# Kernel tuning notes

Hardware: AMD Instinct MI355X
Metric: run time of the kernel (lower is better)

## Reference

```python
import jax, jax.numpy as jnp
from jax import lax
import numpy as np

V, D, L, E = 32000, 256, 4, 4
B, S = 1, 4096  # B must be 1: AstroNorm's buffer update/broadcast only works for batch==1
SIG = float(1.0 / (1.0 + np.exp(-0.15)))        # sigmoid(init_sparsity=0.15), static (int() detaches)
K_GATE = max(1, int(S * SIG))                    # tokens kept by sparsity gate
K_EXP = max(1, int(0.8 * E))                     # int(sparsity_constraint * num_experts) = 3


def setup_inputs() -> dict:
    key = jax.random.key(0)
    ks = jax.random.split(key, 8)
    s = 0.02
    return {
        "tokens": jax.random.randint(ks[0], (B, S), 0, V),
        "emb": jax.random.normal(ks[1], (V, D)) * s,
        "buffers": jax.random.normal(ks[2], (L, D)) * 0.1,   # AstroNorm buffer per layer
        "decays": jnp.full((L,), 0.95),                       # AstroNorm decay per layer
        "gate_w": jax.random.normal(ks[3], (L, D)) * s,       # context_gate (Linear(dim,1,bias=False))
        "gating_W": jax.random.normal(ks[4], (L, E, D)) * s,  # expert router
        "gating_b": jnp.zeros((L, E)),
        "exp_W": jax.random.normal(ks[5], (L, E, D, D)) * s,  # per-expert Linear(dim,dim)
        "exp_b": jnp.zeros((L, E, D)),
        "ln_g": jnp.ones((D,)),
        "ln_b": jnp.zeros((D,)),
        "head_W": jax.random.normal(ks[6], (V, D)) * s,
        "head_b": jnp.zeros((V,)),
    }


def _forward(tokens, emb, buffers, decays, gate_w, gating_W, gating_b,
             exp_W, exp_b, ln_g, ln_b, head_W, head_b):
    x = emb[tokens]  # [B,S,D]
    for l in range(L):
        # ---- AstroNorm: stats over sequence dim (dim=1), detached as in torch ----
        mu = lax.stop_gradient(jnp.mean(x, axis=1, keepdims=True))           # [B,1,D]
        var = lax.stop_gradient(jnp.var(x, axis=1, keepdims=True, ddof=1))   # unbiased var
        new_buf = decays[l] * buffers[l] + (1.0 - decays[l]) * mu.squeeze()  # [D] (B==1)
        x = jnp.where(jnp.abs(x - mu) > jnp.abs(new_buf), mu, x) / jnp.sqrt(var + 1e-6)
        # ---- DynamicSparsityGate: keep tokens strictly above k-th score ----
        scores = jnp.einsum('bsd,d->bs', x, gate_w[l])
        thr = lax.top_k(scores, K_GATE)[0][:, -1:]           # k-th largest per row
        x = x * (scores > thr).astype(x.dtype)[..., None]
        # ---- SparseExpert: top-K_EXP experts per token, masked accumulation ----
        gs = jnp.einsum('bsd,ed->bse', x, gating_W[l]) + gating_b[l]
        idx = lax.top_k(gs, K_EXP)[1]                                    # [B,S,k]
        emask = (jax.nn.one_hot(idx, E).sum(-2) > 0).astype(x.dtype)     # [B,S,E]
        ys = jnp.einsum('bsd,eod->bseo', x, exp_W[l]) + exp_b[l]         # all-expert outputs
        x = jnp.einsum('bse,bseo->bso', emask, ys)
    # ---- LayerNorm (biased var, eps=1e-5) + vocab head ----
    mu = jnp.mean(x, axis=-1, keepdims=True)
    v = jnp.var(x, axis=-1, keepdims=True)
    x = (x - mu) / jnp.sqrt(v + 1e-5) * ln_g + ln_b
    return jnp.einsum('bsd,vd->bsv', x, head_W) + head_b


def reference(tokens, emb, buffers, decays, gate_w, gating_W, gating_b,
              exp_W, exp_b, ln_g, ln_b, head_W, head_b):
    return _forward(tokens, emb, buffers, decays, gate_w, gating_W, gating_b,
                    exp_W, exp_b, ln_g, ln_b, head_W, head_b)
```

## Files before the change

### kernel.cpp

```cpp
#include <hip/hip_runtime.h>
#include <hip/hip_bf16.h>
#include <math.h>

#define V 32000
#define D 256
#define L 4
#define E 4
#define S 4096
#define K_GATE 2201
#define NE 1024
#define NCH 64
#define SCHUNK 64
#define CTS 136


typedef __hip_bfloat16 bf16;
typedef __attribute__((ext_vector_type(8))) short bf16x8;
typedef __attribute__((ext_vector_type(4))) float f32x4;

__device__ __forceinline__ float loadf(const void* p, size_t i, int bf) {
    if (bf) return __bfloat162float(((const bf16*)p)[i]);
    return ((const float*)p)[i];
}

#define GLDS16(g, l)                                                            \
    __builtin_amdgcn_global_load_lds(                                           \
        (const __attribute__((address_space(1))) unsigned int*)(g),             \
        (__attribute__((address_space(3))) unsigned int*)(l), 16, 0, 0)

__device__ __forceinline__ void stage_tile(const bf16* __restrict__ src, int rowStride,
                                           short* lds, int t, int k0) {
    int w = t >> 6, l = t & 63;
    #pragma unroll
    for (int i = 0; i < 2; i++) {
        int chunk = (w * 2 + i) * 64 + l;
        int row = chunk >> 2;
        int c8 = (chunk & 3) ^ ((row >> 1) & 3);
        const bf16* g = src + (size_t)row * rowStride + k0 + c8 * 8;
        GLDS16(g, (char*)lds + (size_t)(w * 2 + i) * 1024);
    }
}

__device__ __forceinline__ bf16x8 frag_ld(const short* lds, int row, int quad) {
    return *(const bf16x8*)&lds[row * 32 + ((quad ^ ((row >> 1) & 3)) << 3)];
}

__global__ void k_detect(const void* __restrict__ emb, int* __restrict__ flag) {
    const unsigned short* h = (const unsigned short*)emb;
    int cnt = 0;
    for (int i = 0; i < 128; i += 2) {
        int e = (h[i] >> 7) & 0xFF;
        if (e >= 100 && e <= 130) cnt++;
    }
    *flag = (cnt >= 32) ? 1 : 0;
}

__global__ void k_wcast(const void* __restrict__ W, const int* __restrict__ bfp,
                        bf16* __restrict__ Wb) {
    if (*bfp) return;
    size_t idx = ((size_t)blockIdx.x * 256 + threadIdx.x) * 4;
    float4 v = *(const float4*)((const float*)W + idx);
    Wb[idx + 0] = __float2bfloat16(v.x);
    Wb[idx + 1] = __float2bfloat16(v.y);
    Wb[idx + 2] = __float2bfloat16(v.z);
    Wb[idx + 3] = __float2bfloat16(v.w);
}

__global__ void k_embed(const int* __restrict__ tok, const void* __restrict__ emb,
                        const int* __restrict__ bfp, float* __restrict__ x) {
    int s = blockIdx.x, d = threadIdx.x;
    int bf = *bfp;
    int t = tok[s];
    x[s * D + d] = loadf(emb, (size_t)t * D + d, bf);
}

__global__ void k_stats_part(const float* __restrict__ x, float* __restrict__ psum,
                             float* __restrict__ psq) {
    int b = blockIdx.x;
    int t = threadIdx.x;
    float s = 0.f, q = 0.f;
    int s0 = b * SCHUNK;
    #pragma unroll 4
    for (int i = 0; i < SCHUNK; i++) {
        float v = x[(size_t)(s0 + i) * D + t];
        s += v; q += v * v;
    }
    psum[b * D + t] = s;
    psq[b * D + t] = q;
}

__global__ void k_stats_fin(const float* __restrict__ psum, const float* __restrict__ psq,
                            const void* __restrict__ buffers, const void* __restrict__ decays,
                            const int* __restrict__ bfp, int l,
                            float* __restrict__ mu, float* __restrict__ rstd,
                            float* __restrict__ absnb) {
    int t = threadIdx.x;
    int bf = *bfp;
    float s = 0.f, q = 0.f;
    for (int b = 0; b < NCH; b++) { s += psum[b * D + t]; q += psq[b * D + t]; }
    float m = s / (float)S;
    float var = (q - (float)S * m * m) / (float)(S - 1);
    float dec = loadf(decays, l, bf);
    float nb = dec * loadf(buffers, l * D + t, bf) + (1.f - dec) * m;
    mu[t] = m;
    rstd[t] = rsqrtf(var + 1e-6f);
    absnb[t] = fabsf(nb);
}

__global__ void k_norm_score(float* __restrict__ x, const float* __restrict__ mu,
                             const float* __restrict__ rstd, const float* __restrict__ absnb,
                             const void* __restrict__ gate_w, const int* __restrict__ bfp,
                             int l, float* __restrict__ scores) {
    int t = threadIdx.x, w = t >> 6, ln = t & 63;
    int s = blockIdx.x * 4 + w;
    int bf = *bfp;
    float part = 0.f;
    #pragma unroll
    for (int j = 0; j < 4; j++) {
        int f = ln + j * 64;
        float m = mu[f];
        float v = x[(size_t)s * D + f];
        float xv = (fabsf(v - m) > absnb[f]) ? m : v;
        xv *= rstd[f];
        x[(size_t)s * D + f] = xv;
        part += xv * loadf(gate_w, l * D + f, bf);
    }
    #pragma unroll
    for (int m2 = 1; m2 < 64; m2 <<= 1) part += __shfl_xor(part, m2, 64);
    if (ln == 0) scores[s] = part;
}

__global__ void k_thr(const float* __restrict__ scores, float* __restrict__ thr) {
    __shared__ unsigned keys[S];
    __shared__ unsigned hist[256];
    __shared__ unsigned scanb[256];
    __shared__ unsigned sh_pref, sh_rank, sh_bucket;
    int t = threadIdx.x;
    for (int i = t; i < S; i += 256) {
        unsigned u = __float_as_uint(scores[i]);
        keys[i] = (u & 0x80000000u) ? ~u : (u | 0x80000000u);
    }
    if (t == 0) { sh_pref = 0u; sh_rank = S - K_GATE; }
    __syncthreads();
    for (int shift = 24; shift >= 0; shift -= 8) {
        unsigned pref = sh_pref, r = sh_rank;
        unsigned pmask = (shift == 24) ? 0u : (0xFFFFFFFFu << (shift + 8));
        hist[t] = 0u;
        __syncthreads();
        for (int i = t; i < S; i += 256) {
            unsigned k = keys[i];
            if ((k & pmask) == pref) atomicAdd(&hist[(k >> shift) & 0xFF], 1u);
        }
        __syncthreads();
        unsigned v = hist[t];
        scanb[t] = v;
        __syncthreads();
        for (int o = 1; o < 256; o <<= 1) {
            unsigned u2 = (t >= o) ? scanb[t - o] : 0u;
            __syncthreads();
            scanb[t] += u2;
            __syncthreads();
        }
        unsigned incl = scanb[t], exc = incl - v;
        if (exc <= r && r < incl) {
            sh_bucket = t;
            sh_rank = r - exc;
        }
        __syncthreads();
        if (t == 0) sh_pref = pref | (sh_bucket << shift);
        __syncthreads();
    }
    if (t == 0) {
        unsigned k = sh_pref;
        unsigned u = (k & 0x80000000u) ? (k ^ 0x80000000u) : ~k;
        thr[0] = __uint_as_float(u);
    }
}

__global__ void k_route(const float* __restrict__ x, const float* __restrict__ scores,
                        const float* __restrict__ thr,
                        const void* __restrict__ gating_W, const void* __restrict__ gating_b,
                        const int* __restrict__ bfp, int l,
                        float* __restrict__ xg, int* __restrict__ excl) {
    int t = threadIdx.x, w = t >> 6, ln = t & 63;
    int s = blockIdx.x * 4 + w;
    int bf = *bfp;
    float keep = (scores[s] > thr[0]) ? 1.f : 0.f;
    float xv[4];
    #pragma unroll
    for (int j = 0; j < 4; j++) {
        int f = ln + j * 64;
        float v = x[(size_t)s * D + f] * keep;
        xv[j] = v;
        xg[(size_t)s * D + f] = v;
    }
    float gs[E];
    #pragma unroll
    for (int e = 0; e < E; e++) {
        float p = 0.f;
        #pragma unroll
        for (int j = 0; j < 4; j++)
            p += xv[j] * loadf(gating_W, (size_t)(l * E + e) * D + ln + j * 64, bf);
        #pragma unroll
        for (int m2 = 1; m2 < 64; m2 <<= 1) p += __shfl_xor(p, m2, 64);
        gs[e] = p + loadf(gating_b, l * E + e, bf);
    }
    if (ln == 0) {
        int mi = 0; float mv = gs[0];
        #pragma unroll
        for (int e = 1; e < E; e++) if (gs[e] <= mv) { mv = gs[e]; mi = e; }
        excl[s] = mi;
    }
}

#define BM 64
#define BN 64
#define BK 32
__global__ __launch_bounds__(256) void k_egemm(const float* __restrict__ xg,
                                               const void* __restrict__ exp_W,
                                               const int* __restrict__ bfp, int l,
                                               float* __restrict__ Y) {
    __shared__ float As[BK][BM + 1];
    __shared__ float Bs[BK][BN + 1];
    int bf = *bfp;
    int bn = blockIdx.x * BN;
    int bm = blockIdx.y * BM;
    int t = threadIdx.x;
    int tm = (t >> 4) << 2;
    int tn = (t & 15) << 2;
    float acc[4][4] = {};
    for (int k0 = 0; k0 < D; k0 += BK) {
        for (int i = t; i < BM * BK; i += 256) {
            int m = i >> 5, k = i & 31;
            As[k][m] = xg[(size_t)(bm + m) * D + k0 + k];
        }
        for (int i = t; i < BN * BK; i += 256) {
            int n = i >> 5, k = i & 31;
            int gn = bn + n;
            int e = gn >> 8, o = gn & 255;
            Bs[k][n] = loadf(exp_W, ((size_t)((l * E + e) * D + o)) * D + k0 + k, bf);
        }
        __syncthreads();
        for (int k = 0; k < BK; k++) {
            float a[4], bb[4];
            #pragma unroll
            for (int i = 0; i < 4; i++) a[i] = As[k][tm + i];
            #pragma unroll
            for (int j = 0; j < 4; j++) bb[j] = Bs[k][tn + j];
            #pragma unroll
            for (int i = 0; i < 4; i++)
                #pragma unroll
                for (int j = 0; j < 4; j++)
                    acc[i][j] += a[i] * bb[j];
        }
        __syncthreads();
    }
    #pragma unroll
    for (int i = 0; i < 4; i++)
        #pragma unroll
        for (int j = 0; j < 4; j++)
            Y[(size_t)(bm + tm + i) * NE + bn + tn + j] = acc[i][j];
}

__global__ void k_combine(const float* __restrict__ Y, const int* __restrict__ excl,
                          const void* __restrict__ exp_b, const int* __restrict__ bfp,
                          int l, float* __restrict__ xo) {
    int s = blockIdx.x, t = threadIdx.x;
    int bf = *bfp;
    int ex = excl[s];
    float a = 0.f;
    for (int e = 0; e < E; e++) {
        if (e == ex) continue;
        a += Y[(size_t)s * NE + e * D + t] + loadf(exp_b, (size_t)(l * E + e) * D + t, bf);
    }
    xo[s * D + t] = a;
}

__global__ void k_ln(const float* __restrict__ x, const void* __restrict__ g,
                     const void* __restrict__ b, const int* __restrict__ bfp,
                     bf16* __restrict__ xnb) {
    int t = threadIdx.x, w = t >> 6, ln = t & 63;
    int s = blockIdx.x * 4 + w;
    int bf = *bfp;
    float vv[4];
    float sum = 0.f, sq = 0.f;
    #pragma unroll
    for (int j = 0; j < 4; j++) {
        float v = x[(size_t)s * D + ln + j * 64];
        vv[j] = v; sum += v; sq += v * v;
    }
    #pragma unroll
    for (int m2 = 1; m2 < 64; m2 <<= 1) {
        sum += __shfl_xor(sum, m2, 64);
        sq  += __shfl_xor(sq, m2, 64);
    }
    float m = sum / (float)D;
    float var = sq / (float)D - m * m;
    float r = rsqrtf(var + 1e-5f);
    #pragma unroll
    for (int j = 0; j < 4; j++) {
        int f = ln + j * 64;
        xnb[(size_t)s * D + f] = __float2bfloat16((vv[j] - m) * r * loadf(g, f, bf)
                                                  + loadf(b, f, bf));
    }
}

__global__ __launch_bounds__(256) void k_head_mfma(const bf16* __restrict__ xnb,
                                                   const void* __restrict__ head_W_raw,
                                                   const bf16* __restrict__ Wb,
                                                   const void* __restrict__ bias,
                                                   const int* __restrict__ bfp,
                                                   void* __restrict__ out) {
    __shared__ __align__(16) char smem[128 * CTS * 2];
    short* At = (short*)smem;
    short* Bt = (short*)(smem + 8192);
    short* Ct = (short*)smem;
    int bf = *bfp;
    const bf16* Wsrc = bf ? (const bf16*)head_W_raw : Wb;
    int bs = blockIdx.x * 128;
    int bv = blockIdx.y * 128;
    int t = threadIdx.x;
    int wave = t >> 6, lane = t & 63;
    int wm = (wave >> 1) * 64, wn = (wave & 1) * 64;
    int quad = lane >> 4, l16 = lane & 15;

    f32x4 acc[4][4] = {};
    for (int k0 = 0; k0 < D; k0 += 32) {
        stage_tile(xnb + (size_t)bs * D, D, At, t, k0);
        stage_tile(Wsrc + (size_t)bv * D, D, Bt, t, k0);
        __syncthreads();
        bf16x8 af[4], bfg[4];
        #pragma unroll
        for (int i = 0; i < 4; i++) af[i]  = frag_ld(At, wm + i * 16 + l16, quad);
        #pragma unroll
        for (int j = 0; j < 4; j++) bfg[j] = frag_ld(Bt, wn + j * 16 + l16, quad);
        #pragma unroll
        for (int i = 0; i < 4; i++)
            #pragma unroll
            for (int j = 0; j < 4; j++)
                acc[i][j] = __builtin_amdgcn_mfma_f32_16x16x32_bf16(af[i], bfg[j], acc[i][j], 0, 0, 0);
        __syncthreads();
    }
    if (bf) {
        #pragma unroll
        for (int j = 0; j < 4; j++) {
            int colL = wn + j * 16 + l16;
            float bb = __bfloat162float(((const bf16*)bias)[bv + colL]);
            #pragma unroll
            for (int i = 0; i < 4; i++) {
                int rowL = wm + i * 16 + quad * 4;
                #pragma unroll
                for (int rg = 0; rg < 4; rg++) {
                    bf16 hv = __float2bfloat16(acc[i][j][rg] + bb);
                    Ct[(rowL + rg) * CTS + colL] = *(short*)&hv;
                }
            }
        }
        __syncthreads();
        bf16* ob = (bf16*)out;
        #pragma unroll
        for (int k = 0; k < 8; k++) {
            int cc = k * 256 + t;
            int row = cc >> 4, c16 = cc & 15;
            bf16x8 v = *(const bf16x8*)&Ct[row * CTS + c16 * 8];
            *(bf16x8*)(ob + (size_t)(bs + row) * V + bv + c16 * 8) = v;
        }
    } else {
        float* of = (float*)out;
        #pragma unroll
        for (int j = 0; j < 4; j++) {
            int col = bv + wn + j * 16 + l16;
            float bb = loadf(bias, col, bf);
            #pragma unroll
            for (int i = 0; i < 4; i++) {
                int row0 = bs + wm + i * 16 + quad * 4;
                #pragma unroll
                for (int rg = 0; rg < 4; rg++)
                    of[(size_t)(row0 + rg) * V + col] = acc[i][j][rg] + bb;
            }
        }
    }
}

extern "C" void kernel_launch(void* const* d_in, const int* in_sizes, int n_in,
                              void* d_out, int out_size, void* d_ws, size_t ws_size,
                              hipStream_t stream) {
    const int*  tokens   = (const int*)d_in[0];
    const void* emb      = d_in[1];
    const void* buffers  = d_in[2];
    const void* decays   = d_in[3];
    const void* gate_w   = d_in[4];
    const void* gating_W = d_in[5];
    const void* gating_b = d_in[6];
    const void* exp_W    = d_in[7];
    const void* exp_b    = d_in[8];
    const void* ln_g     = d_in[9];
    const void* ln_b     = d_in[10];
    const void* head_W   = d_in[11];
    const void* head_b   = d_in[12];

    char* p = (char*)d_ws;
    bf16* Wb    = (bf16*)p;             p += (size_t)V * D * 2;
    bf16* xnb   = (bf16*)p;             p += (size_t)S * D * 2;
    float* xA   = (float*)p;            p += (size_t)S * D * 4;
    float* xB   = (float*)p;            p += (size_t)S * D * 4;
    float* xg   = (float*)p;            p += (size_t)S * D * 4;
    float* Y    = (float*)p;            p += (size_t)S * NE * 4;
    float* psum = (float*)p;            p += (size_t)NCH * D * 4;
    float* psq  = (float*)p;            p += (size_t)NCH * D * 4;
    float* scores = (float*)p;          p += (size_t)S * 4;
    float* mu   = (float*)p;            p += D * 4;
    float* rstd = (float*)p;            p += D * 4;
    float* absnb = (float*)p;           p += D * 4;
    float* thr  = (float*)p;            p += 16;
    int* flag   = (int*)p;              p += 16;
    int* excl   = (int*)p;              p += (size_t)S * 4;

    k_detect<<<1, 1, 0, stream>>>(emb, flag);
    k_wcast<<<(V * D) / 1024, 256, 0, stream>>>(head_W, flag, Wb);
    k_embed<<<S, D, 0, stream>>>(tokens, emb, flag, xA);

    float* xc = xA;
    float* xo = xB;
    for (int l = 0; l < L; l++) {
        k_stats_part<<<NCH, 256, 0, stream>>>(xc, psum, psq);
        k_stats_fin<<<1, 256, 0, stream>>>(psum, psq, buffers, decays, flag, l, mu, rstd, absnb);
        k_norm_score<<<S / 4, 256, 0, stream>>>(xc, mu, rstd, absnb, gate_w, flag, l, scores);
        k_thr<<<1, 256, 0, stream>>>(scores, thr);
        k_route<<<S / 4, 256, 0, stream>>>(xc, scores, thr, gating_W, gating_b, flag, l,
                                           xg, excl);
        dim3 ge(NE / BN, S / BM);
        k_egemm<<<ge, 256, 0, stream>>>(xg, exp_W, flag, l, Y);
        k_combine<<<S, 256, 0, stream>>>(Y, excl, exp_b, flag, l, xo);
        float* tmp = xc; xc = xo; xo = tmp;
    }
    k_ln<<<S / 4, 256, 0, stream>>>(xc, ln_g, ln_b, flag, xnb);
    dim3 gh(S / 128, V / 128);
    k_head_mfma<<<gh, 256, 0, stream>>>(xnb, head_W, Wb, head_b, flag, d_out);
}
```

Measured before the change: 1.180 ms.

## Fuse routing into expert GEMM and combine, enlarge GEMM tiles, speed up threshold select

Removes the separate routing kernel. The sparsity mask is now applied while staging A tiles in the expert GEMM, and the router logits plus excluded-expert choice are computed inside the combine kernel, which drops the xg and excl buffers and one launch per layer. The FP32 expert GEMM moves from 64x64 to 128x128 tiles with 8x8 per-thread outputs and vectorized loads and stores, raising arithmetic intensity at the cost of more registers and fewer blocks. The radix threshold kernel now runs 1024 threads and replaces the barrier-heavy shared-memory scan with a single-wave shuffle scan.

Result: faster. 991.7 us (-16.0%).

```diff
diff --git a/kernel.cpp b/kernel.cpp
--- a/kernel.cpp
+++ b/kernel.cpp
@@ -22,6 +22,9 @@
     if (bf) return __bfloat162float(((const bf16*)p)[i]);
     return ((const float*)p)[i];
 }
+__device__ __forceinline__ float us2f(unsigned short u) {
+    return __uint_as_float((unsigned)u << 16);
+}
 
 #define GLDS16(g, l)                                                            \
     __builtin_amdgcn_global_load_lds(                                           \
@@ -133,38 +136,52 @@
 __global__ void k_thr(const float* __restrict__ scores, float* __restrict__ thr) {
     __shared__ unsigned keys[S];
     __shared__ unsigned hist[256];
-    __shared__ unsigned scanb[256];
     __shared__ unsigned sh_pref, sh_rank, sh_bucket;
     int t = threadIdx.x;
-    for (int i = t; i < S; i += 256) {
-        unsigned u = __float_as_uint(scores[i]);
-        keys[i] = (u & 0x80000000u) ? ~u : (u | 0x80000000u);
+    #pragma unroll
+    for (int i = 0; i < 4; i++) {
+        int idx = i * 1024 + t;
+        unsigned u = __float_as_uint(scores[idx]);
+        keys[idx] = (u & 0x80000000u) ? ~u : (u | 0x80000000u);
     }
     if (t == 0) { sh_pref = 0u; sh_rank = S - K_GATE; }
     __syncthreads();
     for (int shift = 24; shift >= 0; shift -= 8) {
+        if (t < 256) hist[t] = 0u;
+        __syncthreads();
         unsigned pref = sh_pref, r = sh_rank;
         unsigned pmask = (shift == 24) ? 0u : (0xFFFFFFFFu << (shift + 8));
-        hist[t] = 0u;
-        __syncthreads();
-        for (int i = t; i < S; i += 256) {
-            unsigned k = keys[i];
+        #pragma unroll
+        for (int i = 0; i < 4; i++) {
+            unsigned k = keys[i * 1024 + t];
             if ((k & pmask) == pref) atomicAdd(&hist[(k >> shift) & 0xFF], 1u);
         }
         __syncthreads();
-        unsigned v = hist[t];
-        scanb[t] = v;
-        __syncthreads();
-        for (int o = 1; o < 256; o <<= 1) {
-            unsigned u2 = (t >= o) ? scanb[t - o] : 0u;
-            __syncthreads();
-            scanb[t] += u2;
-            __syncthreads();
-        }
-        unsigned incl = scanb[t], exc = incl - v;
-        if (exc <= r && r < incl) {
-            sh_bucket = t;
-            sh_rank = r - exc;
+        if (t < 64) {
+            unsigned h[4];
+            unsigned loc = 0u;
+            #pragma unroll
+            for (int j = 0; j < 4; j++) { h[j] = hist[t * 4 + j]; loc += h[j]; }
+            unsigned pre = loc;
+            #pragma unroll
+            for (int off = 1; off < 64; off <<= 1) {
+                unsigned u2 = __shfl_up(pre, off, 64);
+                if (t >= off) pre += u2;
+            }
+            unsigned base = pre - loc;
+            if (r >= base && r < pre) {
+                unsigned rr = r - base;
+                int bsel = -1;
+                #pragma unroll
+                for (int j = 0; j < 4; j++) {
+                    if (bsel < 0) {
+                        if (rr < h[j]) bsel = j;
+                        else rr -= h[j];
+                    }
+                }
+                sh_bucket = (unsigned)(t * 4 + bsel);
+                sh_rank = rr;
+            }
         }
         __syncthreads();
         if (t == 0) sh_pref = pref | (sh_bucket << shift);
@@ -177,103 +194,138 @@
     }
 }
 
-__global__ void k_route(const float* __restrict__ x, const float* __restrict__ scores,
-                        const float* __restrict__ thr,
-                        const void* __restrict__ gating_W, const void* __restrict__ gating_b,
-                        const int* __restrict__ bfp, int l,
-                        float* __restrict__ xg, int* __restrict__ excl) {
-    int t = threadIdx.x, w = t >> 6, ln = t & 63;
-    int s = blockIdx.x * 4 + w;
-    int bf = *bfp;
-    float keep = (scores[s] > thr[0]) ? 1.f : 0.f;
-    float xv[4];
-    #pragma unroll
-    for (int j = 0; j < 4; j++) {
-        int f = ln + j * 64;
-        float v = x[(size_t)s * D + f] * keep;
-        xv[j] = v;
-        xg[(size_t)s * D + f] = v;
-    }
-    float gs[E];
-    #pragma unroll
-    for (int e = 0; e < E; e++) {
-        float p = 0.f;
-        #pragma unroll
-        for (int j = 0; j < 4; j++)
-            p += xv[j] * loadf(gating_W, (size_t)(l * E + e) * D + ln + j * 64, bf);
-        #pragma unroll
-        for (int m2 = 1; m2 < 64; m2 <<= 1) p += __shfl_xor(p, m2, 64);
-        gs[e] = p + loadf(gating_b, l * E + e, bf);
-    }
-    if (ln == 0) {
-        int mi = 0; float mv = gs[0];
-        #pragma unroll
-        for (int e = 1; e < E; e++) if (gs[e] <= mv) { mv = gs[e]; mi = e; }
-        excl[s] = mi;
-    }
-}
-
-#define BM 64
-#define BN 64
-#define BK 32
-__global__ __launch_bounds__(256) void k_egemm(const float* __restrict__ xg,
+#define EBM 128
+#define EBN 128
+#define EBK 32
+__global__ __launch_bounds__(256) void k_egemm(const float* __restrict__ x,
+                                               const float* __restrict__ scores,
+                                               const float* __restrict__ thr,
                                                const void* __restrict__ exp_W,
                                                const int* __restrict__ bfp, int l,
                                                float* __restrict__ Y) {
-    __shared__ float As[BK][BM + 1];
-    __shared__ float Bs[BK][BN + 1];
-    int bf = *bfp;
-    int bn = blockIdx.x * BN;
-    int bm = blockIdx.y * BM;
+    __shared__ float As[EBK][EBM + 4];
+    __shared__ float Bs[EBK][EBN + 4];
+    __shared__ float kp[EBM];
+    int bf = *bfp;
+    int bn = blockIdx.x * EBN;
+    int bm = blockIdx.y * EBM;
     int t = threadIdx.x;
-    int tm = (t >> 4) << 2;
-    int tn = (t & 15) << 2;
-    float acc[4][4] = {};
-    for (int k0 = 0; k0 < D; k0 += BK) {
-        for (int i = t; i < BM * BK; i += 256) {
-            int m = i >> 5, k = i & 31;
-            As[k][m] = xg[(size_t)(bm + m) * D + k0 + k];
-        }
-        for (int i = t; i < BN * BK; i += 256) {
-            int n = i >> 5, k = i & 31;
-            int gn = bn + n;
-            int e = gn >> 8, o = gn & 255;
-            Bs[k][n] = loadf(exp_W, ((size_t)((l * E + e) * D + o)) * D + k0 + k, bf);
-        }
-        __syncthreads();
-        for (int k = 0; k < BK; k++) {
-            float a[4], bb[4];
-            #pragma unroll
-            for (int i = 0; i < 4; i++) a[i] = As[k][tm + i];
-            #pragma unroll
-            for (int j = 0; j < 4; j++) bb[j] = Bs[k][tn + j];
-            #pragma unroll
-            for (int i = 0; i < 4; i++)
+    int tm = (t >> 4) * 8;
+    int tn = (t & 15) * 8;
+    if (t < EBM) kp[t] = (scores[bm + t] > thr[0]) ? 1.f : 0.f;
+    __syncthreads();
+    const unsigned short* Wb16 = (const unsigned short*)exp_W;
+    const float* Wf32 = (const float*)exp_W;
+    size_t wbase = (size_t)l * NE * D;
+    float acc[8][8] = {};
+    for (int k0 = 0; k0 < D; k0 += EBK) {
+        #pragma unroll
+        for (int i = 0; i < 4; i++) {
+            int chunk = i * 256 + t;
+            int m = chunk >> 3, c4 = chunk & 7;
+            float4 v = *(const float4*)&x[(size_t)(bm + m) * D + k0 + c4 * 4];
+            float kk = kp[m];
+            As[c4 * 4 + 0][m] = v.x * kk;
+            As[c4 * 4 + 1][m] = v.y * kk;
+            As[c4 * 4 + 2][m] = v.z * kk;
+            As[c4 * 4 + 3][m] = v.w * kk;
+        }
+        if (bf) {
+            #pragma unroll
+            for (int i = 0; i < 2; i++) {
+                int chunk = i * 256 + t;
+                int n = chunk >> 2, c8 = chunk & 3;
+                const unsigned short* src = Wb16 + wbase + (size_t)(bn + n) * D + k0 + c8 * 8;
+                ushort4 v0 = *(const ushort4*)src;
+                ushort4 v1 = *(const ushort4*)(src + 4);
+                Bs[c8 * 8 + 0][n] = us2f(v0.x);
+                Bs[c8 * 8 + 1][n] = us2f(v0.y);
+                Bs[c8 * 8 + 2][n] = us2f(v0.z);
+                Bs[c8 * 8 + 3][n] = us2f(v0.w);
+                Bs[c8 * 8 + 4][n] = us2f(v1.x);
+                Bs[c8 * 8 + 5][n] = us2f(v1.y);
+                Bs[c8 * 8 + 6][n] = us2f(v1.z);
+                Bs[c8 * 8 + 7][n] = us2f(v1.w);
+            }
+        } else {
+            #pragma unroll
+            for (int i = 0; i < 4; i++) {
+                int chunk = i * 256 + t;
+                int n = chunk >> 3, c4 = chunk & 7;
+                float4 v = *(const float4*)&Wf32[wbase + (size_t)(bn + n) * D + k0 + c4 * 4];
+                Bs[c4 * 4 + 0][n] = v.x;
+                Bs[c4 * 4 + 1][n] = v.y;
+                Bs[c4 * 4 + 2][n] = v.z;
+                Bs[c4 * 4 + 3][n] = v.w;
+            }
+        }
+        __syncthreads();
+        #pragma unroll 4
+        for (int k = 0; k < EBK; k++) {
+            float a[8], b[8];
+            *(float4*)&a[0] = *(const float4*)&As[k][tm];
+            *(float4*)&a[4] = *(const float4*)&As[k][tm + 4];
+            *(float4*)&b[0] = *(const float4*)&Bs[k][tn];
+            *(float4*)&b[4] = *(const float4*)&Bs[k][tn + 4];
+            #pragma unroll
+            for (int i = 0; i < 8; i++)
                 #pragma unroll
-                for (int j = 0; j < 4; j++)
-                    acc[i][j] += a[i] * bb[j];
-        }
-        __syncthreads();
-    }
-    #pragma unroll
-    for (int i = 0; i < 4; i++)
+                for (int j = 0; j < 8; j++)
+                    acc[i][j] += a[i] * b[j];
+        }
+        __syncthreads();
+    }
+    #pragma unroll
+    for (int i = 0; i < 8; i++) {
+        float4 o0 = { acc[i][0], acc[i][1], acc[i][2], acc[i][3] };
+        float4 o1 = { acc[i][4], acc[i][5], acc[i][6], acc[i][7] };
+        float* dst = &Y[(size_t)(bm + tm + i) * NE + bn + tn];
+        *(float4*)dst = o0;
+        *(float4*)(dst + 4) = o1;
+    }
+}
+
+__global__ void k_comb(const float* __restrict__ x, const float* __restrict__ scores,
+                       const float* __restrict__ thr,
+                       const void* __restrict__ gating_W, const void* __restrict__ gating_b,
+                       const float* __restrict__ Y, const void* __restrict__ exp_b,
+                       const int* __restrict__ bfp, int l, float* __restrict__ xo) {
+    int t = threadIdx.x, w = t >> 6, ln = t & 63;
+    int s = blockIdx.x * 4 + w;
+    int bf = *bfp;
+    float keep = (scores[s] > thr[0]) ? 1.f : 0.f;
+    float xv[4];
+    #pragma unroll
+    for (int j = 0; j < 4; j++)
+        xv[j] = x[(size_t)s * D + ln + j * 64] * keep;
+    float gs[E];
+    #pragma unroll
+    for (int e = 0; e < E; e++) {
+        float p = 0.f;
         #pragma unroll
         for (int j = 0; j < 4; j++)
-            Y[(size_t)(bm + tm + i) * NE + bn + tn + j] = acc[i][j];
-}
-
-__global__ void k_combine(const float* __restrict__ Y, const int* __restrict__ excl,
-                          const void* __restrict__ exp_b, const int* __restrict__ bfp,
-                          int l, float* __restrict__ xo) {
-    int s = blockIdx.x, t = threadIdx.x;
-    int bf = *bfp;
-    int ex = excl[s];
-    float a = 0.f;
-    for (int e = 0; e < E; e++) {
-        if (e == ex) continue;
-        a += Y[(size_t)s * NE + e * D + t] + loadf(exp_b, (size_t)(l * E + e) * D + t, bf);
-    }
-    xo[s * D + t] = a;
+            p += xv[j] * loadf(gating_W, (size_t)(l * E + e) * D + ln + j * 64, bf);
+        #pragma unroll
+        for (int m2 = 1; m2 < 64; m2 <<= 1) p += __shfl_xor(p, m2, 64);
+        gs[e] = p + loadf(gating_b, l * E + e, bf);
+    }
+    int mi = 0;
+    if (ln == 0) {
+        float mv = gs[0];
+        #pragma unroll
+        for (int e = 1; e < E; e++) if (gs[e] <= mv) { mv = gs[e]; mi = e; }
+    }
+    int excl = __shfl(mi, 0, 64);
+    #pragma unroll
+    for (int j = 0; j < 4; j++) {
+        int f = ln + j * 64;
+        float a = 0.f;
+        for (int e = 0; e < E; e++) {
+            if (e == excl) continue;
+            a += Y[(size_t)s * NE + e * D + f] + loadf(exp_b, (size_t)(l * E + e) * D + f, bf);
+        }
+        xo[(size_t)s * D + f] = a;
+    }
 }
 
 __global__ void k_ln(const float* __restrict__ x, const void* __restrict__ g,
@@ -404,7 +456,6 @@
     bf16* xnb   = (bf16*)p;             p += (size_t)S * D * 2;
     float* xA   = (float*)p;            p += (size_t)S * D * 4;
     float* xB   = (float*)p;            p += (size_t)S * D * 4;
-    float* xg   = (float*)p;            p += (size_t)S * D * 4;
     float* Y    = (float*)p;            p += (size_t)S * NE * 4;
     float* psum = (float*)p;            p += (size_t)NCH * D * 4;
     float* psq  = (float*)p;            p += (size_t)NCH * D * 4;
@@ -414,7 +465,6 @@
     float* absnb = (float*)p;           p += D * 4;
     float* thr  = (float*)p;            p += 16;
     int* flag   = (int*)p;              p += 16;
-    int* excl   = (int*)p;              p += (size_t)S * 4;
 
     k_detect<<<1, 1, 0, stream>>>(emb, flag);
     k_wcast<<<(V * D) / 1024, 256, 0, stream>>>(head_W, flag, Wb);
@@ -426,12 +476,11 @@
         k_stats_part<<<NCH, 256, 0, stream>>>(xc, psum, psq);
         k_stats_fin<<<1, 256, 0, stream>>>(psum, psq, buffers, decays, flag, l, mu, rstd, absnb);
         k_norm_score<<<S / 4, 256, 0, stream>>>(xc, mu, rstd, absnb, gate_w, flag, l, scores);
-        k_thr<<<1, 256, 0, stream>>>(scores, thr);
-        k_route<<<S / 4, 256, 0, stream>>>(xc, scores, thr, gating_W, gating_b, flag, l,
-                                           xg, excl);
-        dim3 ge(NE / BN, S / BM);
-        k_egemm<<<ge, 256, 0, stream>>>(xg, exp_W, flag, l, Y);
-        k_combine<<<S, 256, 0, stream>>>(Y, excl, exp_b, flag, l, xo);
+        k_thr<<<1, 1024, 0, stream>>>(scores, thr);
+        dim3 ge(NE / EBN, S / EBM);
+        k_egemm<<<ge, 256, 0, stream>>>(xc, scores, thr, exp_W, flag, l, Y);
+        k_comb<<<S / 4, 256, 0, stream>>>(xc, scores, thr, gating_W, gating_b, Y,
+                                          exp_b, flag, l, xo);
         float* tmp = xc; xc = xo; xo = tmp;
     }
     k_ln<<<S / 4, 256, 0, stream>>>(xc, ln_g, ln_b, flag, xnb);
```
